# Optimization experiments

Measured on AMD Instinct MI355X. Metric: run time of the kernel, lower is better.

The kernel has to match this reference:

```python
import jax, jax.numpy as jnp
import numpy as np

D_MODEL = 1024
NUM_HEADS = 16
DEPTH = D_MODEL // NUM_HEADS
B, S = 2, 2048


def setup_inputs() -> dict:
    key = jax.random.key(0)
    ks = jax.random.split(key, 11)
    scale = 1.0 / np.sqrt(D_MODEL)
    inp = {
        "v": jax.random.normal(ks[0], (B, S, D_MODEL), dtype=jnp.float32),
        "k": jax.random.normal(ks[1], (B, S, D_MODEL), dtype=jnp.float32),
        "q": jax.random.normal(ks[2], (B, S, D_MODEL), dtype=jnp.float32),
        "wq": jax.random.normal(ks[3], (D_MODEL, D_MODEL), dtype=jnp.float32) * scale,
        "bq": jnp.zeros((D_MODEL,), dtype=jnp.float32),
        "wk": jax.random.normal(ks[4], (D_MODEL, D_MODEL), dtype=jnp.float32) * scale,
        "bk": jnp.zeros((D_MODEL,), dtype=jnp.float32),
        "wv": jax.random.normal(ks[5], (D_MODEL, D_MODEL), dtype=jnp.float32) * scale,
        "bv": jnp.zeros((D_MODEL,), dtype=jnp.float32),
        "wo": jax.random.normal(ks[6], (D_MODEL, D_MODEL), dtype=jnp.float32) * scale,
        "bo": jnp.zeros((D_MODEL,), dtype=jnp.float32),
    }
    return inp


def _split_heads(x):
    # (B, S, D) -> (B, H, S, depth)
    b, s, _ = x.shape
    return x.reshape(b, s, NUM_HEADS, DEPTH).transpose(0, 2, 1, 3)


def reference(v, k, q, wq, bq, wk, bk, wv, bv, wo, bo):
    qh = _split_heads(q @ wq + bq)  # (B,H,S,d)
    kh = _split_heads(k @ wk + bk)
    vh = _split_heads(v @ wv + bv)
    scores = jnp.einsum("bhqd,bhkd->bhqk", qh, kh) / jnp.sqrt(
        jnp.asarray(DEPTH, dtype=qh.dtype))
    attn = jax.nn.softmax(scores, axis=-1)
    out = jnp.einsum("bhqk,bhkd->bhqd", attn, vh)  # (B,H,S,d)
    out = out.transpose(0, 2, 1, 3).reshape(q.shape[0], -1, D_MODEL)
    return out @ wo + bo
```

## Files before the change

### kernel.cpp

```cpp
#include <hip/hip_runtime.h>
#include <hip/hip_bf16.h>

#define S_LEN 2048
#define DM 1024
#define NH 16
#define DH 64
#define MROWS 4096

typedef __hip_bfloat16 hbf;
typedef __attribute__((ext_vector_type(4))) float floatx4;
typedef __bf16 bf16x8 __attribute__((ext_vector_type(8)));

#define QSCALE 0.18033688f


__global__ __launch_bounds__(256) void cvt3w(
    const float* __restrict__ q, const float* __restrict__ k, const float* __restrict__ v,
    hbf* __restrict__ Xqh, hbf* __restrict__ Xkh, hbf* __restrict__ Xvh,
    const float* __restrict__ wq, const float* __restrict__ wk,
    const float* __restrict__ wv, const float* __restrict__ wo,
    hbf* __restrict__ Wqh, hbf* __restrict__ Wkh,
    hbf* __restrict__ Wvh, hbf* __restrict__ Woh) {
  __shared__ float tile[64][65];
  const int t = threadIdx.x;
  if (blockIdx.y < 3) {
    const float* src; hbf* dst;
    switch (blockIdx.y) {
      case 0:  src = q; dst = Xqh; break;
      case 1:  src = k; dst = Xkh; break;
      default: src = v; dst = Xvh; break;
    }
    const int mt = blockIdx.x >> 4, kt = blockIdx.x & 15;
    const int s0 = mt * 64, k0 = kt * 64;
    const int lanep = t & 63, l15p = lanep & 15, quadp = lanep >> 4;
#pragma unroll
    for (int it = 0; it < 2; ++it) {
      int fl = (t >> 6) * 2 + it;
      int fm = fl >> 1, fk = fl & 1;
      const float* rp = &src[(size_t)(s0 + fm * 16 + l15p) * DM + k0 + fk * 32 + quadp * 8];
      const float4 v0 = *(const float4*)rp;
      const float4 v1 = *(const float4*)(rp + 4);
      union { hbf h[8]; uint4 u; } pk;
      pk.h[0] = __float2bfloat16(v0.x); pk.h[1] = __float2bfloat16(v0.y);
      pk.h[2] = __float2bfloat16(v0.z); pk.h[3] = __float2bfloat16(v0.w);
      pk.h[4] = __float2bfloat16(v1.x); pk.h[5] = __float2bfloat16(v1.y);
      pk.h[6] = __float2bfloat16(v1.z); pk.h[7] = __float2bfloat16(v1.w);
      size_t base = ((size_t)(mt * 4 + fm) * 32 + (kt * 2 + fk)) * 512 + lanep * 8;
      *(uint4*)&dst[base] = pk.u;
    }
    return;
  }
  const float* W; hbf* Wh;
  switch (blockIdx.x >> 8) {
    case 0:  W = wq; Wh = Wqh; break;
    case 1:  W = wk; Wh = Wkh; break;
    case 2:  W = wv; Wh = Wvh; break;
    default: W = wo; Wh = Woh; break;
  }
  const int t8 = blockIdx.x & 255;
  const int n0 = (t8 & 15) * 64, k0 = (t8 >> 4) * 64;
  const int c4 = (t & 15) * 4, r16 = t >> 4;
#pragma unroll
  for (int i = 0; i < 4; ++i) {
    int row = i * 16 + r16;
    const float4 vv = *(const float4*)&W[(size_t)(k0 + row) * DM + n0 + c4];
    tile[row][c4 + 0] = vv.x; tile[row][c4 + 1] = vv.y;
    tile[row][c4 + 2] = vv.z; tile[row][c4 + 3] = vv.w;
  }
  __syncthreads();
  {
    const int lane = t & 63, l15w = lane & 15, quadw = lane >> 4, wv_ = t >> 6;
    const int nnl = wv_ * 16 + l15w;
#pragma unroll
    for (int j = 0; j < 2; ++j) {
      const int kk0 = j * 32 + quadw * 8;
      union { hbf h[8]; uint4 u; } pk;
#pragma unroll
      for (int e = 0; e < 8; ++e)
        pk.h[e] = __float2bfloat16(tile[kk0 + e][nnl]);
      size_t base = ((size_t)((n0 + nnl) >> 4) * 32 + ((k0 + kk0) >> 5)) * 512 + lane * 8;
      *(uint4*)&Wh[base] = pk.u;
    }
  }
}

__global__ __launch_bounds__(256) void gemm_qkv(
    const hbf* __restrict__ Xqh, const hbf* __restrict__ Xkh, const hbf* __restrict__ Xvh,
    const hbf* __restrict__ Wqh, const hbf* __restrict__ Wkh, const hbf* __restrict__ Wvh,
    const float* __restrict__ bq, const float* __restrict__ bk, const float* __restrict__ bv,
    hbf* __restrict__ Qh, hbf* __restrict__ Kf, hbf* __restrict__ Vf) {
  const int id = blockIdx.x;
  const int x = id & 7, idx = id >> 3;
  const int z = idx >> 5, rem = idx & 31;
  const int nblk = rem >> 1, mblk = rem & 1;

  const hbf* Ah; const hbf* Bh; const float* bias; hbf* Out; float oscale;
  if (z == 0)      { Ah = Xqh; Bh = Wqh; bias = bq; Out = Qh; oscale = QSCALE; }
  else if (z == 1) { Ah = Xkh; Bh = Wkh; bias = bk; Out = Kf; oscale = 1.0f; }
  else             { Ah = Xvh; Bh = Wvh; bias = bv; Out = Vf; oscale = 1.0f; }

  const int tid = threadIdx.x;
  const int lane = tid & 63, wave = tid >> 6;
  const int l15 = lane & 15, quad = lane >> 4;
  const int M0 = x * 512 + mblk * 256 + wave * 64;
  const int n0 = nblk * 64;

  const hbf* ap = Ah + (size_t)(M0 >> 4) * 32 * 512 + lane * 8;
  const hbf* bp = Bh + (size_t)(n0 >> 4) * 32 * 512 + lane * 8;

  floatx4 acc[4][4] = {};
  bf16x8 a0[4], b0[4], a1[4], b1[4];
#pragma unroll
  for (int i = 0; i < 4; ++i) {
    a0[i] = *(const bf16x8*)&ap[(size_t)i * 16384];
    b0[i] = *(const bf16x8*)&bp[(size_t)i * 16384];
  }

#pragma unroll 1
  for (int kb = 0; kb < 32; kb += 2) {
#pragma unroll
    for (int i = 0; i < 4; ++i) {
      a1[i] = *(const bf16x8*)&ap[(size_t)i * 16384 + (kb + 1) * 512];
      b1[i] = *(const bf16x8*)&bp[(size_t)i * 16384 + (kb + 1) * 512];
    }
    __builtin_amdgcn_s_setprio(1);
#pragma unroll
    for (int mi = 0; mi < 4; ++mi)
#pragma unroll
      for (int ni = 0; ni < 4; ++ni)
        acc[mi][ni] = __builtin_amdgcn_mfma_f32_16x16x32_bf16(a0[mi], b0[ni], acc[mi][ni], 0, 0, 0);
    __builtin_amdgcn_s_setprio(0);
    const int k2 = kb + 2;
    if (k2 < 32) {
#pragma unroll
      for (int i = 0; i < 4; ++i) {
        a0[i] = *(const bf16x8*)&ap[(size_t)i * 16384 + k2 * 512];
        b0[i] = *(const bf16x8*)&bp[(size_t)i * 16384 + k2 * 512];
      }
    }
    __builtin_amdgcn_s_setprio(1);
#pragma unroll
    for (int mi = 0; mi < 4; ++mi)
#pragma unroll
      for (int ni = 0; ni < 4; ++ni)
        acc[mi][ni] = __builtin_amdgcn_mfma_f32_16x16x32_bf16(a1[mi], b1[ni], acc[mi][ni], 0, 0, 0);
    __builtin_amdgcn_s_setprio(0);
  }

#pragma unroll
  for (int mi = 0; mi < 4; ++mi) {
#pragma unroll
    for (int ni = 0; ni < 4; ++ni) {
      int col = n0 + ni * 16 + l15;
      float bb_ = bias[col];
#pragma unroll
      for (int r = 0; r < 4; ++r) {
        int row = M0 + mi * 16 + quad * 4 + r;
        float vv = (acc[mi][ni][r] + bb_) * oscale;
        int b = row >> 11, s = row & 2047, h = col >> 6, dd = col & 63;
        int bh = b * NH + h;
        size_t idxo;
        if (z == 1) {
          int kt = s >> 5, nif = (s >> 4) & 1, fl15 = s & 15;
          int ksf = dd >> 5, fquad = (dd >> 3) & 3, e = dd & 7;
          idxo = (((size_t)bh * 64 + kt) * 4 + ksf * 2 + nif) * 512 + (fquad * 16 + fl15) * 8 + e;
        } else if (z == 2) {
          int kt = s >> 5, u = s & 31;
          int p = 2 * (u & 15) + (u >> 4);
          int fquad = p >> 3, e = p & 7;
          int nd = dd >> 4, fl15 = dd & 15;
          idxo = (((size_t)bh * 64 + kt) * 4 + nd) * 512 + (fquad * 16 + fl15) * 8 + e;
        } else {
          idxo = (((size_t)bh * S_LEN + s) << 6) + dd;
        }
        Out[idxo] = __float2bfloat16(vv);
      }
    }
  }
}

__global__ __launch_bounds__(256, 4) void flash_attn(
    const hbf* __restrict__ Qh, const hbf* __restrict__ Kf,
    const hbf* __restrict__ Vf, hbf* __restrict__ AO) {
  const int id = blockIdx.x;
  const int bh = (id & 7) * 4 + (id >> 8);
  const int q0 = ((id >> 3) & 31) * 64;
  const int b = bh >> 4, h = bh & 15;
  const int tid = threadIdx.x;
  const int lane = tid & 63, wave = tid >> 6;
  const int qw = wave & 1;
  const int ksplit = wave >> 1;
  const int l15 = lane & 15, quad = lane >> 4;

  __shared__ __align__(16) unsigned char smem[17408];
  __shared__ float Lbuf[2][32];
  hbf* Pw = (hbf*)(smem + wave * 2560);

  const size_t qbase = (((size_t)bh) * S_LEN + q0 + qw * 32) * DH;
  bf16x8 qf[2][2];
#pragma unroll
  for (int mi = 0; mi < 2; ++mi)
#pragma unroll
    for (int ks = 0; ks < 2; ++ks)
      qf[mi][ks] = *(const bf16x8*)&Qh[qbase + (size_t)(mi * 16 + l15) * DH + ks * 32 + quad * 8];

  bf16x8 ones_f;
  {
    const __bf16 ov = (l15 == 0) ? (__bf16)1.0f : (__bf16)0.0f;
#pragma unroll
    for (int j = 0; j < 8; ++j) ones_f[j] = ov;
  }

  floatx4 o[2][4] = {};
  floatx4 lsum[2] = {};

  const hbf* Kb = Kf + ((size_t)bh * 64 + ksplit * 32) * 2048 + lane * 8;
  const hbf* Vb = Vf + ((size_t)bh * 64 + ksplit * 32) * 2048 + lane * 8;

  bf16x8 kf[2][2], vf[4];
#pragma unroll
  for (int ni = 0; ni < 2; ++ni)
#pragma unroll
    for (int ks = 0; ks < 2; ++ks)
      kf[ni][ks] = *(const bf16x8*)&Kb[(ks * 2 + ni) * 512];
#pragma unroll
  for (int nd = 0; nd < 4; ++nd)
    vf[nd] = *(const bf16x8*)&Vb[nd * 512];

#pragma unroll 1
  for (int it = 0; it < 32; ++it) {
    const int tn = (it + 1) * 2048;

    floatx4 sacc[2][2] = {};
    __builtin_amdgcn_s_setprio(1);
#pragma unroll
    for (int ks = 0; ks < 2; ++ks)
#pragma unroll
      for (int mi = 0; mi < 2; ++mi)
#pragma unroll
        for (int ni = 0; ni < 2; ++ni)
          sacc[mi][ni] = __builtin_amdgcn_mfma_f32_16x16x32_bf16(qf[mi][ks], kf[ni][ks], sacc[mi][ni], 0, 0, 0);
    __builtin_amdgcn_s_setprio(0);

    if (it < 31) {
#pragma unroll
      for (int ni = 0; ni < 2; ++ni)
#pragma unroll
        for (int ks = 0; ks < 2; ++ks)
          kf[ni][ks] = *(const bf16x8*)&Kb[tn + (ks * 2 + ni) * 512];
    }

#pragma unroll
    for (int mi = 0; mi < 2; ++mi)
#pragma unroll
      for (int r = 0; r < 4; ++r) {
        union { hbf h2[2]; unsigned int u; } pk2;
        pk2.h2[0] = __float2bfloat16(__builtin_amdgcn_exp2f(sacc[mi][0][r]));
        pk2.h2[1] = __float2bfloat16(__builtin_amdgcn_exp2f(sacc[mi][1][r]));
        *(unsigned int*)&Pw[(mi * 16 + quad * 4 + r) * 40 + 2 * l15] = pk2.u;
      }

    bf16x8 pf[2];
#pragma unroll
    for (int mi = 0; mi < 2; ++mi)
      pf[mi] = *(const bf16x8*)&Pw[(mi * 16 + l15) * 40 + quad * 8];

    __builtin_amdgcn_s_setprio(1);
#pragma unroll
    for (int mi = 0; mi < 2; ++mi)
      lsum[mi] = __builtin_amdgcn_mfma_f32_16x16x32_bf16(pf[mi], ones_f, lsum[mi], 0, 0, 0);

#pragma unroll
    for (int nd = 0; nd < 4; ++nd)
#pragma unroll
      for (int mi = 0; mi < 2; ++mi)
        o[mi][nd] = __builtin_amdgcn_mfma_f32_16x16x32_bf16(pf[mi], vf[nd], o[mi][nd], 0, 0, 0);
    __builtin_amdgcn_s_setprio(0);

    if (it < 31) {
#pragma unroll
      for (int nd = 0; nd < 4; ++nd)
        vf[nd] = *(const bf16x8*)&Vb[tn + nd * 512];
    }
  }

  __syncthreads();
  if (ksplit == 1) {
    float* Ob = (float*)smem + qw * (32 * 68);
#pragma unroll
    for (int mi = 0; mi < 2; ++mi)
#pragma unroll
      for (int nd = 0; nd < 4; ++nd)
#pragma unroll
        for (int r = 0; r < 4; ++r)
          Ob[(mi * 16 + quad * 4 + r) * 68 + nd * 16 + l15] = o[mi][nd][r];
    if (l15 == 0) {
#pragma unroll
      for (int mi = 0; mi < 2; ++mi)
#pragma unroll
        for (int r = 0; r < 4; ++r)
          Lbuf[qw][mi * 16 + quad * 4 + r] = lsum[mi][r];
    }
  }
  __syncthreads();
  if (ksplit == 0) {
    const float* Ob = (const float*)smem + qw * (32 * 68);
#pragma unroll
    for (int mi = 0; mi < 2; ++mi) {
      float linv[4];
#pragma unroll
      for (int r = 0; r < 4; ++r) {
        float lq = __shfl(lsum[mi][r], lane & 48, 64) + Lbuf[qw][mi * 16 + quad * 4 + r];
        linv[r] = 1.0f / lq;
      }
      const int m16 = (b * S_LEN + q0 + qw * 32 + mi * 16) >> 4;
#pragma unroll
      for (int nd = 0; nd < 4; ++nd) {
        const int kb = h * 2 + (nd >> 1);
        const int qa = ((nd & 1) << 1) + (l15 >> 3);
        const int dd = nd * 16 + l15;
#pragma unroll
        for (int r = 0; r < 4; ++r) {
          int rl = mi * 16 + quad * 4 + r;
          float vv = (o[mi][nd][r] + Ob[rl * 68 + dd]) * linv[r];
          size_t idxo = ((size_t)m16 * 32 + kb) * 512 + (qa * 16 + quad * 4 + r) * 8 + (l15 & 7);
          AO[idxo] = __float2bfloat16(vv);
        }
      }
    }
  }
}

__global__ __launch_bounds__(256) void gemm_out(
    const hbf* __restrict__ Ah, const hbf* __restrict__ Bh,
    const float* __restrict__ bias, float* __restrict__ Out) {
  const int id = blockIdx.x;
  const int x = id & 7, idx = id >> 3;
  const int nblk = idx >> 3, mblk = idx & 7;
  const int tid = threadIdx.x;
  const int lane = tid & 63, wave = tid >> 6;
  const int l15 = lane & 15, quad = lane >> 4;
  const int wm = wave >> 1, wn = wave & 1;
  const int M0 = x * 512 + mblk * 64 + wm * 32;
  const int n0 = nblk * 128 + wn * 64;

  const hbf* ap = Ah + (size_t)(M0 >> 4) * 32 * 512 + lane * 8;
  const hbf* bp = Bh + (size_t)(n0 >> 4) * 32 * 512 + lane * 8;

  floatx4 acc[2][4] = {};
  bf16x8 a0[2], b0[4], a1[2], b1[4];
#pragma unroll
  for (int i = 0; i < 2; ++i) a0[i] = *(const bf16x8*)&ap[(size_t)i * 16384];
#pragma unroll
  for (int i = 0; i < 4; ++i) b0[i] = *(const bf16x8*)&bp[(size_t)i * 16384];

#pragma unroll 1
  for (int kb = 0; kb < 32; kb += 2) {
#pragma unroll
    for (int i = 0; i < 2; ++i) a1[i] = *(const bf16x8*)&ap[(size_t)i * 16384 + (kb + 1) * 512];
#pragma unroll
    for (int i = 0; i < 4; ++i) b1[i] = *(const bf16x8*)&bp[(size_t)i * 16384 + (kb + 1) * 512];
    __builtin_amdgcn_s_setprio(1);
#pragma unroll
    for (int mi = 0; mi < 2; ++mi)
#pragma unroll
      for (int ni = 0; ni < 4; ++ni)
        acc[mi][ni] = __builtin_amdgcn_mfma_f32_16x16x32_bf16(a0[mi], b0[ni], acc[mi][ni], 0, 0, 0);
    __builtin_amdgcn_s_setprio(0);
    const int k2 = kb + 2;
    if (k2 < 32) {
#pragma unroll
      for (int i = 0; i < 2; ++i) a0[i] = *(const bf16x8*)&ap[(size_t)i * 16384 + k2 * 512];
#pragma unroll
      for (int i = 0; i < 4; ++i) b0[i] = *(const bf16x8*)&bp[(size_t)i * 16384 + k2 * 512];
    }
    __builtin_amdgcn_s_setprio(1);
#pragma unroll
    for (int mi = 0; mi < 2; ++mi)
#pragma unroll
      for (int ni = 0; ni < 4; ++ni)
        acc[mi][ni] = __builtin_amdgcn_mfma_f32_16x16x32_bf16(a1[mi], b1[ni], acc[mi][ni], 0, 0, 0);
    __builtin_amdgcn_s_setprio(0);
  }

#pragma unroll
  for (int mi = 0; mi < 2; ++mi) {
#pragma unroll
    for (int ni = 0; ni < 4; ++ni) {
      int col = n0 + ni * 16 + l15;
      float bb_ = bias[col];
#pragma unroll
      for (int r = 0; r < 4; ++r) {
        int row = M0 + mi * 16 + quad * 4 + r;
        Out[(size_t)row * DM + col] = acc[mi][ni][r] + bb_;
      }
    }
  }
}

extern "C" void kernel_launch(void* const* d_in, const int* in_sizes, int n_in,
                              void* d_out, int out_size, void* d_ws, size_t ws_size,
                              hipStream_t stream) {
  const float* v  = (const float*)d_in[0];
  const float* k  = (const float*)d_in[1];
  const float* q  = (const float*)d_in[2];
  const float* wq = (const float*)d_in[3];
  const float* bq = (const float*)d_in[4];
  const float* wk = (const float*)d_in[5];
  const float* bk = (const float*)d_in[6];
  const float* wv = (const float*)d_in[7];
  const float* bv = (const float*)d_in[8];
  const float* wo = (const float*)d_in[9];
  const float* bo = (const float*)d_in[10];

  const size_t NX = (size_t)MROWS * DM;
  const size_t NW = (size_t)DM * DM;
  hbf* base = (hbf*)d_ws;
  hbf* Xqh = base;
  hbf* Xkh = Xqh + NX;
  hbf* Xvh = Xkh + NX;
  hbf* Wqh = Xvh + NX;
  hbf* Wkh = Wqh + NW;
  hbf* Wvh = Wkh + NW;
  hbf* Woh = Wvh + NW;
  hbf* Qh  = Woh + NW;
  hbf* Kf  = Qh + NX;
  hbf* Vf  = Kf + NX;
  hbf* AOh = Vf + NX;

  cvt3w<<<dim3(1024, 4), 256, 0, stream>>>(q, k, v, Xqh, Xkh, Xvh,
                                           wq, wk, wv, wo, Wqh, Wkh, Wvh, Woh);
  gemm_qkv<<<768, 256, 0, stream>>>(Xqh, Xkh, Xvh, Wqh, Wkh, Wvh, bq, bk, bv, Qh, Kf, Vf);
  flash_attn<<<1024, 256, 0, stream>>>(Qh, Kf, Vf, AOh);
  gemm_out<<<512, 256, 0, stream>>>(AOh, Woh, bo, (float*)d_out);
}
```

Baseline: 229.2 us.

## Stage QKV GEMM tiles through LDS with async global-to-LDS double buffering

The QKV projection GEMM now uses 128x128 block tiles with a 2x2 wave layout instead of four waves each streaming their own A/B fragments from global memory. Operands are staged in shared memory using global_load_lds, double-buffered across k-steps, so each loaded fragment is shared by two waves. This halves redundant global/L2 traffic per block. In exchange it adds a __syncthreads per k-step and LDS pressure, and the register prefetch pipeline is gone.

After: 216.9 us. 5.3% less time.

```diff
diff --git a/kernel.cpp b/kernel.cpp
--- a/kernel.cpp
+++ b/kernel.cpp
@@ -12,6 +12,10 @@
 typedef __bf16 bf16x8 __attribute__((ext_vector_type(8)));
 
 #define QSCALE 0.18033688f
+
+#define GLOAD_LDS(g, l) __builtin_amdgcn_global_load_lds(                      \
+    (const __attribute__((address_space(1))) void*)(g),                        \
+    (__attribute__((address_space(3))) void*)(l), 16, 0, 0)
 
 
 __global__ __launch_bounds__(256) void cvt3w(
@@ -92,7 +96,7 @@
   const int id = blockIdx.x;
   const int x = id & 7, idx = id >> 3;
   const int z = idx >> 5, rem = idx & 31;
-  const int nblk = rem >> 1, mblk = rem & 1;
+  const int nblk = rem >> 2, mblk = rem & 3;
 
   const hbf* Ah; const hbf* Bh; const float* bias; hbf* Out; float oscale;
   if (z == 0)      { Ah = Xqh; Bh = Wqh; bias = bq; Out = Qh; oscale = QSCALE; }
@@ -101,50 +105,57 @@
 
   const int tid = threadIdx.x;
   const int lane = tid & 63, wave = tid >> 6;
+  const int wm = wave >> 1, wn = wave & 1;
   const int l15 = lane & 15, quad = lane >> 4;
-  const int M0 = x * 512 + mblk * 256 + wave * 64;
-  const int n0 = nblk * 64;
-
-  const hbf* ap = Ah + (size_t)(M0 >> 4) * 32 * 512 + lane * 8;
-  const hbf* bp = Bh + (size_t)(n0 >> 4) * 32 * 512 + lane * 8;
+  const int M0 = x * 512 + mblk * 128 + wm * 64;
+  const int n0 = nblk * 128 + wn * 64;
+
+  __shared__ __align__(16) hbf As[2][8][512];
+  __shared__ __align__(16) hbf Bs[2][8][512];
+
+  const int sf = (wave & 1) * 4;
+  const bool isB = wave >= 2;
+  const int mt16 = (x * 512 + mblk * 128) >> 4;
+  const int nt16 = (nblk * 128) >> 4;
+  const hbf* gbase = isB ? Bh + (size_t)(nt16 + sf) * 32 * 512 + lane * 8
+                         : Ah + (size_t)(mt16 + sf) * 32 * 512 + lane * 8;
+
+#pragma unroll
+  for (int f = 0; f < 4; ++f) {
+    const hbf* g = gbase + (size_t)f * 16384;
+    if (isB) GLOAD_LDS(g, &Bs[0][sf + f][0]);
+    else     GLOAD_LDS(g, &As[0][sf + f][0]);
+  }
+  __syncthreads();
 
   floatx4 acc[4][4] = {};
-  bf16x8 a0[4], b0[4], a1[4], b1[4];
-#pragma unroll
-  for (int i = 0; i < 4; ++i) {
-    a0[i] = *(const bf16x8*)&ap[(size_t)i * 16384];
-    b0[i] = *(const bf16x8*)&bp[(size_t)i * 16384];
-  }
-
+  int buf = 0;
 #pragma unroll 1
-  for (int kb = 0; kb < 32; kb += 2) {
+  for (int kb = 0; kb < 32; ++kb) {
+    if (kb < 31) {
+      const int nb = buf ^ 1;
+#pragma unroll
+      for (int f = 0; f < 4; ++f) {
+        const hbf* g = gbase + (size_t)f * 16384 + (size_t)(kb + 1) * 512;
+        if (isB) GLOAD_LDS(g, &Bs[nb][sf + f][0]);
+        else     GLOAD_LDS(g, &As[nb][sf + f][0]);
+      }
+    }
+    bf16x8 a[4], b[4];
 #pragma unroll
     for (int i = 0; i < 4; ++i) {
-      a1[i] = *(const bf16x8*)&ap[(size_t)i * 16384 + (kb + 1) * 512];
-      b1[i] = *(const bf16x8*)&bp[(size_t)i * 16384 + (kb + 1) * 512];
+      a[i] = *(const bf16x8*)&As[buf][wm * 4 + i][lane * 8];
+      b[i] = *(const bf16x8*)&Bs[buf][wn * 4 + i][lane * 8];
     }
     __builtin_amdgcn_s_setprio(1);
 #pragma unroll
     for (int mi = 0; mi < 4; ++mi)
 #pragma unroll
       for (int ni = 0; ni < 4; ++ni)
-        acc[mi][ni] = __builtin_amdgcn_mfma_f32_16x16x32_bf16(a0[mi], b0[ni], acc[mi][ni], 0, 0, 0);
+        acc[mi][ni] = __builtin_amdgcn_mfma_f32_16x16x32_bf16(a[mi], b[ni], acc[mi][ni], 0, 0, 0);
     __builtin_amdgcn_s_setprio(0);
-    const int k2 = kb + 2;
-    if (k2 < 32) {
-#pragma unroll
-      for (int i = 0; i < 4; ++i) {
-        a0[i] = *(const bf16x8*)&ap[(size_t)i * 16384 + k2 * 512];
-        b0[i] = *(const bf16x8*)&bp[(size_t)i * 16384 + k2 * 512];
-      }
-    }
-    __builtin_amdgcn_s_setprio(1);
-#pragma unroll
-    for (int mi = 0; mi < 4; ++mi)
-#pragma unroll
-      for (int ni = 0; ni < 4; ++ni)
-        acc[mi][ni] = __builtin_amdgcn_mfma_f32_16x16x32_bf16(a1[mi], b1[ni], acc[mi][ni], 0, 0, 0);
-    __builtin_amdgcn_s_setprio(0);
+    __syncthreads();
+    buf ^= 1;
   }
 
 #pragma unroll
```
